# Kernel tuning notes

Hardware: AMD Instinct MI355X
Metric: run time of the kernel (lower is better)

The kernel has to match this reference:

```python
import jax, jax.numpy as jnp
import numpy as np

N_NODES = 50000
N_EDGES = 600000
IN_DIM, HID_DIM, OUT_DIM = 128, 256, 40


def setup_inputs() -> dict:
    key = jax.random.key(0)
    ks = jax.random.split(key, 10)
    x = jax.random.normal(ks[0], (N_NODES, IN_DIM), dtype=jnp.float32)
    edge_index = jax.random.randint(ks[1], (2, N_EDGES), 0, N_NODES, dtype=jnp.int64)
    def lin(k, out_d, in_d):
        s = 1.0 / np.sqrt(in_d)
        return jax.random.uniform(k, (out_d, in_d), jnp.float32, -s, s)
    # SAGEConv: lin_l (on aggregated neighbors, with bias) + lin_r (on self, no bias)
    params = {
        "Wl1": lin(ks[2], HID_DIM, IN_DIM), "bl1": jnp.zeros((HID_DIM,), jnp.float32), "Wr1": lin(ks[3], HID_DIM, IN_DIM),
        "Wl2": lin(ks[4], HID_DIM, HID_DIM), "bl2": jnp.zeros((HID_DIM,), jnp.float32), "Wr2": lin(ks[5], HID_DIM, HID_DIM),
        "Wl3": lin(ks[6], OUT_DIM, HID_DIM), "bl3": jnp.zeros((OUT_DIM,), jnp.float32), "Wr3": lin(ks[7], OUT_DIM, HID_DIM),
    }
    return {"x": x, "edge_index": edge_index, **params}


def _sage_conv(x, src, dst, Wl, bl, Wr):
    # mean-aggregate source features into destination nodes
    n = x.shape[0]
    agg = jax.ops.segment_sum(x[src], dst, num_segments=n)          # [N, d_in]
    cnt = jax.ops.segment_sum(jnp.ones_like(dst, dtype=x.dtype), dst, num_segments=n)
    mean = agg / jnp.maximum(cnt, 1.0)[:, None]
    return mean @ Wl.T + bl + x @ Wr.T


def reference(x, edge_index, Wl1, bl1, Wr1, Wl2, bl2, Wr2, Wl3, bl3, Wr3):
    src, dst = edge_index[0], edge_index[1]
    h = _sage_conv(x, src, dst, Wl1, bl1, Wr1)
    h = jax.nn.relu(h)  # dropout is identity in eval mode
    h = _sage_conv(h, src, dst, Wl2, bl2, Wr2)
    h = jax.nn.relu(h)
    h = _sage_conv(h, src, dst, Wl3, bl3, Wr3)
    return jax.nn.log_softmax(h, axis=1)
```

## Files before the change

### kernel.cpp

```cpp
#include <hip/hip_runtime.h>
#include <hip/hip_bf16.h>

#define IN_DIM 128
#define HID_DIM 256
#define OUT_DIM 40
#define SCAN_CHUNK 2048

typedef __attribute__((ext_vector_type(8))) __bf16 bf16x8;
typedef __attribute__((ext_vector_type(4))) float f32x4;

__device__ inline ushort f2bf(float f) {
    uint u = __builtin_bit_cast(uint, f);
    u = (u + 0x7fff + ((u >> 16) & 1)) >> 16;
    return (ushort)u;
}
__device__ inline float bfl(uint u) { return __builtin_bit_cast(float, u << 16); }
__device__ inline float bfh(uint u) { return __builtin_bit_cast(float, u & 0xffff0000u); }

__global__ __launch_bounds__(256) void cvt_x(const float* __restrict__ in,
                                             ushort* __restrict__ out, int n4) {
    int i = blockIdx.x * 256 + threadIdx.x;
    if (i < n4) {
        float4 v = ((const float4*)in)[i];
        uint2 o;
        o.x = (uint)f2bf(v.x) | ((uint)f2bf(v.y) << 16);
        o.y = (uint)f2bf(v.z) | ((uint)f2bf(v.w) << 16);
        ((uint2*)out)[i] = o;
    }
}

__global__ __launch_bounds__(256) void cvt_w2(const float* __restrict__ wl,
                                              const float* __restrict__ wr,
                                              ushort* __restrict__ ol,
                                              ushort* __restrict__ orr,
                                              int O, int OPAD, int K) {
    int idx = blockIdx.x * 256 + threadIdx.x;
    int tot = OPAD * K;
    if (idx >= tot) return;
    int row = idx / K;
    int col = idx - row * K;
    ushort vl = 0, vr = 0;
    if (row < O) {
        vl = f2bf(wl[row * K + col]);
        vr = f2bf(wr[row * K + col]);
    }
    ol[idx] = vl;
    orr[idx] = vr;
}

__global__ __launch_bounds__(256) void hist_kernel(const int* __restrict__ dst,
                                                   int* __restrict__ cnt, int E) {
    int e = blockIdx.x * 256 + threadIdx.x;
    if (e < E) atomicAdd(&cnt[dst[e]], 1);
}

__global__ __launch_bounds__(256) void scan_pass1(const int* __restrict__ cnt,
                                                  int* __restrict__ bsum, int N) {
    __shared__ int red[256];
    const int base = blockIdx.x * SCAN_CHUNK;
    int s = 0;
    for (int i = threadIdx.x; i < SCAN_CHUNK; i += 256) {
        int idx = base + i;
        if (idx < N) s += cnt[idx];
    }
    red[threadIdx.x] = s;
    __syncthreads();
    for (int o = 128; o > 0; o >>= 1) {
        if (threadIdx.x < o) red[threadIdx.x] += red[threadIdx.x + o];
        __syncthreads();
    }
    if (threadIdx.x == 0) bsum[blockIdx.x] = red[0];
}

__global__ __launch_bounds__(256) void scan_pass2(int* __restrict__ bsum, int B) {
    __shared__ int ls[256];
    const int t = threadIdx.x;
    int v = (t < B) ? bsum[t] : 0;
    ls[t] = v;
    __syncthreads();
    for (int o = 1; o < 256; o <<= 1) {
        int u = (t >= o) ? ls[t - o] : 0;
        __syncthreads();
        ls[t] += u;
        __syncthreads();
    }
    if (t < B) bsum[t] = ls[t] - v;
}

__global__ __launch_bounds__(256) void scan_pass3(const int* __restrict__ cnt,
                                                  const int* __restrict__ bsum,
                                                  int* __restrict__ rowptr,
                                                  int* __restrict__ cursor,
                                                  float* __restrict__ inv, int N, int E) {
    __shared__ int ls[256];
    const int tbase = blockIdx.x * SCAN_CHUNK + threadIdx.x * 8;
    int c[8];
    int s = 0;
#pragma unroll
    for (int j = 0; j < 8; ++j) {
        int idx = tbase + j;
        c[j] = (idx < N) ? cnt[idx] : 0;
        s += c[j];
    }
    ls[threadIdx.x] = s;
    __syncthreads();
    for (int o = 1; o < 256; o <<= 1) {
        int u = (threadIdx.x >= o) ? ls[threadIdx.x - o] : 0;
        __syncthreads();
        ls[threadIdx.x] += u;
        __syncthreads();
    }
    int run = bsum[blockIdx.x] + ls[threadIdx.x] - s;
#pragma unroll
    for (int j = 0; j < 8; ++j) {
        int idx = tbase + j;
        if (idx < N) {
            rowptr[idx] = run;
            cursor[idx] = run;
            inv[idx] = 1.0f / fmaxf((float)c[j], 1.0f);
            run += c[j];
        }
    }
    if (blockIdx.x == 0 && threadIdx.x == 0) rowptr[N] = E;
}

__global__ __launch_bounds__(256) void fill_kernel(const int* __restrict__ src,
                                                   const int* __restrict__ dst,
                                                   int* __restrict__ cursor,
                                                   int* __restrict__ srcs, int E) {
    int e = blockIdx.x * 256 + threadIdx.x;
    if (e < E) {
        int pos = atomicAdd(&cursor[dst[e]], 1);
        srcs[pos] = src[e];
    }
}

template <int D>
__global__ __launch_bounds__(256) void gather_mean_bf(const ushort* __restrict__ feat,
                                                      const int* __restrict__ rowptr,
                                                      const int* __restrict__ srcs,
                                                      const float* __restrict__ inv,
                                                      ushort* __restrict__ out, int N) {
    constexpr int V = D / 64;
    const int wave = threadIdx.x >> 6;
    const int lane = threadIdx.x & 63;
    const int n = blockIdx.x * 4 + wave;
    if (n >= N) return;
    const int beg = rowptr[n];
    const int end = rowptr[n + 1];
    const int col = lane * V;
    float a0 = 0.f, a1 = 0.f, a2 = 0.f, a3 = 0.f;
    int e = beg;
    if constexpr (V == 4) {
        for (; e + 3 < end; e += 4) {
            int s0 = srcs[e], s1 = srcs[e + 1], s2 = srcs[e + 2], s3 = srcs[e + 3];
            uint2 q0 = *(const uint2*)&feat[(long long)s0 * D + col];
            uint2 q1 = *(const uint2*)&feat[(long long)s1 * D + col];
            uint2 q2 = *(const uint2*)&feat[(long long)s2 * D + col];
            uint2 q3 = *(const uint2*)&feat[(long long)s3 * D + col];
            a0 += (bfl(q0.x) + bfl(q1.x)) + (bfl(q2.x) + bfl(q3.x));
            a1 += (bfh(q0.x) + bfh(q1.x)) + (bfh(q2.x) + bfh(q3.x));
            a2 += (bfl(q0.y) + bfl(q1.y)) + (bfl(q2.y) + bfl(q3.y));
            a3 += (bfh(q0.y) + bfh(q1.y)) + (bfh(q2.y) + bfh(q3.y));
        }
        for (; e + 1 < end; e += 2) {
            int s0 = srcs[e], s1 = srcs[e + 1];
            uint2 q0 = *(const uint2*)&feat[(long long)s0 * D + col];
            uint2 q1 = *(const uint2*)&feat[(long long)s1 * D + col];
            a0 += bfl(q0.x) + bfl(q1.x);
            a1 += bfh(q0.x) + bfh(q1.x);
            a2 += bfl(q0.y) + bfl(q1.y);
            a3 += bfh(q0.y) + bfh(q1.y);
        }
        if (e < end) {
            uint2 q0 = *(const uint2*)&feat[(long long)srcs[e] * D + col];
            a0 += bfl(q0.x); a1 += bfh(q0.x); a2 += bfl(q0.y); a3 += bfh(q0.y);
        }
        const float sc = inv[n];
        uint2 o;
        o.x = (uint)f2bf(a0 * sc) | ((uint)f2bf(a1 * sc) << 16);
        o.y = (uint)f2bf(a2 * sc) | ((uint)f2bf(a3 * sc) << 16);
        *(uint2*)&out[(long long)n * D + col] = o;
    } else {
        for (; e + 3 < end; e += 4) {
            int s0 = srcs[e], s1 = srcs[e + 1], s2 = srcs[e + 2], s3 = srcs[e + 3];
            uint q0 = *(const uint*)&feat[(long long)s0 * D + col];
            uint q1 = *(const uint*)&feat[(long long)s1 * D + col];
            uint q2 = *(const uint*)&feat[(long long)s2 * D + col];
            uint q3 = *(const uint*)&feat[(long long)s3 * D + col];
            a0 += (bfl(q0) + bfl(q1)) + (bfl(q2) + bfl(q3));
            a1 += (bfh(q0) + bfh(q1)) + (bfh(q2) + bfh(q3));
        }
        for (; e + 1 < end; e += 2) {
            int s0 = srcs[e], s1 = srcs[e + 1];
            uint q0 = *(const uint*)&feat[(long long)s0 * D + col];
            uint q1 = *(const uint*)&feat[(long long)s1 * D + col];
            a0 += bfl(q0) + bfl(q1);
            a1 += bfh(q0) + bfh(q1);
        }
        if (e < end) {
            uint q0 = *(const uint*)&feat[(long long)srcs[e] * D + col];
            a0 += bfl(q0); a1 += bfh(q0);
        }
        const float sc = inv[n];
        uint o = (uint)f2bf(a0 * sc) | ((uint)f2bf(a1 * sc) << 16);
        *(uint*)&out[(long long)n * D + col] = o;
    }
}

template <int K, bool RELU, bool OUTBF>
__global__ __launch_bounds__(256, 3) void sage_gemm_mfma(const ushort* __restrict__ Amean,
                                                         const ushort* __restrict__ Aself,
                                                         const ushort* __restrict__ Wl,
                                                         const float* __restrict__ bias,
                                                         const ushort* __restrict__ Wr,
                                                         void* __restrict__ outv, int N, int O) {
    constexpr int KP = K + 8;
    constexpr int NK = K / 32;
    __shared__ __align__(16) ushort Ws[64 * KP];

    const int tid = threadIdx.x;
    const int wave = tid >> 6;
    const int lane = tid & 63;
    const int ln = lane & 15;
    const int quad = lane >> 4;
    const int bm0 = blockIdx.x * 128;
    const int bn0 = blockIdx.y * 64;

    int arow[2];
#pragma unroll
    for (int rt = 0; rt < 2; ++rt) {
        int r = bm0 + wave * 32 + rt * 16 + ln;
        arow[rt] = min(r, N - 1);
    }

    f32x4 acc[2][4] = {};

    for (int phase = 0; phase < 2; ++phase) {
        const ushort* __restrict__ A = phase ? Aself : Amean;
        const ushort* __restrict__ W = phase ? Wr : Wl;

        __syncthreads();
#pragma unroll
        for (int i = tid; i < 64 * (K / 8); i += 256) {
            int row = i / (K / 8);
            int c8 = (i % (K / 8)) * 8;
            *(ulonglong2*)&Ws[row * KP + c8] =
                *(const ulonglong2*)&W[(long long)(bn0 + row) * K + c8];
        }
        __syncthreads();

        bf16x8 areg[NK][2];
#pragma unroll
        for (int kk = 0; kk < NK; ++kk)
#pragma unroll
            for (int rt = 0; rt < 2; ++rt)
                areg[kk][rt] = *(const bf16x8*)&A[(long long)arow[rt] * K + kk * 32 + quad * 8];

#pragma unroll
        for (int kk = 0; kk < NK; ++kk) {
#pragma unroll
            for (int ct = 0; ct < 4; ++ct) {
                bf16x8 b = *(const bf16x8*)&Ws[(ct * 16 + ln) * KP + kk * 32 + quad * 8];
#pragma unroll
                for (int rt = 0; rt < 2; ++rt)
                    acc[rt][ct] = __builtin_amdgcn_mfma_f32_16x16x32_bf16(areg[kk][rt], b, acc[rt][ct], 0, 0, 0);
            }
        }
    }

#pragma unroll
    for (int rt = 0; rt < 2; ++rt) {
        int rbase = bm0 + wave * 32 + rt * 16 + quad * 4;
#pragma unroll
        for (int ct = 0; ct < 4; ++ct) {
            int col = bn0 + ct * 16 + ln;
            if (col >= O) continue;
            float bv = bias[col];
#pragma unroll
            for (int r = 0; r < 4; ++r) {
                int row = rbase + r;
                if (row >= N) continue;
                float v = acc[rt][ct][r] + bv;
                if (RELU) v = fmaxf(v, 0.f);
                if (OUTBF)
                    ((ushort*)outv)[(long long)row * O + col] = f2bf(v);
                else
                    ((float*)outv)[(long long)row * O + col] = v;
            }
        }
    }
}

template <int K>
__global__ __launch_bounds__(256, 3) void sage_gemm_pre(const ushort* __restrict__ A0,
                                                        const ushort* __restrict__ Wl,
                                                        const ushort* __restrict__ Wr,
                                                        ushort* __restrict__ P,
                                                        float* __restrict__ S, int N, int O) {
    constexpr int KP = 2 * K + 8;
    constexpr int NK = K / 32;
    __shared__ __align__(16) ushort Ws[48 * KP];

    const int tid = threadIdx.x;
    const int wave = tid >> 6;
    const int lane = tid & 63;
    const int ln = lane & 15;
    const int quad = lane >> 4;
    const int bm0 = blockIdx.x * 64;

    const int arow = min(bm0 + wave * 16 + ln, N - 1);

#pragma unroll
    for (int i = tid; i < 48 * (K / 8); i += 256) {
        int row = i / (K / 8);
        int c8 = (i % (K / 8)) * 8;
        *(ulonglong2*)&Ws[row * KP + c8] =
            *(const ulonglong2*)&Wl[(long long)row * K + c8];
        *(ulonglong2*)&Ws[row * KP + K + c8] =
            *(const ulonglong2*)&Wr[(long long)row * K + c8];
    }
    __syncthreads();

    bf16x8 areg[NK];
#pragma unroll
    for (int kk = 0; kk < NK; ++kk)
        areg[kk] = *(const bf16x8*)&A0[(long long)arow * K + kk * 32 + quad * 8];

#pragma unroll
    for (int phase = 0; phase < 2; ++phase) {
        f32x4 acc[3] = {};
#pragma unroll
        for (int kk = 0; kk < NK; ++kk) {
#pragma unroll
            for (int ct = 0; ct < 3; ++ct) {
                bf16x8 b = *(const bf16x8*)&Ws[(ct * 16 + ln) * KP + phase * K + kk * 32 + quad * 8];
                acc[ct] = __builtin_amdgcn_mfma_f32_16x16x32_bf16(areg[kk], b, acc[ct], 0, 0, 0);
            }
        }
        int rbase = bm0 + wave * 16 + quad * 4;
#pragma unroll
        for (int ct = 0; ct < 3; ++ct) {
            int col = ct * 16 + ln;
            if (col >= O) continue;
#pragma unroll
            for (int r = 0; r < 4; ++r) {
                int row = rbase + r;
                if (row >= N) continue;
                if (phase == 0)
                    P[(long long)row * O + col] = f2bf(acc[ct][r]);
                else
                    S[(long long)row * O + col] = acc[ct][r];
            }
        }
    }
}

__global__ __launch_bounds__(256) void agg_bias_lsm(const ushort* __restrict__ P,
                                                    const float* __restrict__ S,
                                                    const float* __restrict__ bias,
                                                    const int* __restrict__ rowptr,
                                                    const int* __restrict__ srcs,
                                                    const float* __restrict__ inv,
                                                    float* __restrict__ out, int N) {
    const int wave = threadIdx.x >> 6;
    const int lane = threadIdx.x & 63;
    const int n = blockIdx.x * 4 + wave;
    if (n >= N) return;
    const int beg = rowptr[n];
    const int end = rowptr[n + 1];
    const bool act = lane < OUT_DIM;
    const int cidx = act ? lane : 0;

    float acc = 0.f;
    int e = beg;
    for (; e + 3 < end; e += 4) {
        int s0 = srcs[e], s1 = srcs[e + 1], s2 = srcs[e + 2], s3 = srcs[e + 3];
        float v0 = __builtin_bit_cast(float, (uint)P[(long long)s0 * OUT_DIM + cidx] << 16);
        float v1 = __builtin_bit_cast(float, (uint)P[(long long)s1 * OUT_DIM + cidx] << 16);
        float v2 = __builtin_bit_cast(float, (uint)P[(long long)s2 * OUT_DIM + cidx] << 16);
        float v3 = __builtin_bit_cast(float, (uint)P[(long long)s3 * OUT_DIM + cidx] << 16);
        acc += (v0 + v1) + (v2 + v3);
    }
    for (; e < end; ++e)
        acc += __builtin_bit_cast(float, (uint)P[(long long)srcs[e] * OUT_DIM + cidx] << 16);

    float v = act ? (acc * inv[n] + S[(long long)n * OUT_DIM + lane] + bias[lane]) : -INFINITY;
    float m = v;
#pragma unroll
    for (int o = 32; o > 0; o >>= 1) m = fmaxf(m, __shfl_xor(m, o, 64));
    float ex = act ? expf(v - m) : 0.f;
    float sm = ex;
#pragma unroll
    for (int o = 32; o > 0; o >>= 1) sm += __shfl_xor(sm, o, 64);
    float ls = logf(sm);
    if (act) out[(long long)n * OUT_DIM + lane] = v - m - ls;
}

extern "C" void kernel_launch(void* const* d_in, const int* in_sizes, int n_in,
                              void* d_out, int out_size, void* d_ws, size_t ws_size,
                              hipStream_t stream) {
    const float* x   = (const float*)d_in[0];
    const int*   ei  = (const int*)d_in[1];
    const float* Wl1 = (const float*)d_in[2];
    const float* bl1 = (const float*)d_in[3];
    const float* Wr1 = (const float*)d_in[4];
    const float* Wl2 = (const float*)d_in[5];
    const float* bl2 = (const float*)d_in[6];
    const float* Wr2 = (const float*)d_in[7];
    const float* Wl3 = (const float*)d_in[8];
    const float* bl3 = (const float*)d_in[9];
    const float* Wr3 = (const float*)d_in[10];
    float* out = (float*)d_out;

    const int N = in_sizes[0] / IN_DIM;
    const int E = in_sizes[1] / 2;
    const int* src = ei;
    const int* dst = ei + E;

    char* w = (char*)d_ws;
    size_t off = 0;
    auto alloc = [&](size_t bytes) {
        void* p = w + off;
        off = (off + bytes + 255) & ~(size_t)255;
        return p;
    };
    ushort* xb   = (ushort*)alloc((size_t)N * IN_DIM * 2);
    ushort* M    = (ushort*)alloc((size_t)N * HID_DIM * 2);
    ushort* H1   = (ushort*)alloc((size_t)N * HID_DIM * 2);
    ushort* H2   = (ushort*)alloc((size_t)N * HID_DIM * 2);
    ushort* P3   = (ushort*)alloc((size_t)N * OUT_DIM * 2);
    float*  S3   = (float*)alloc((size_t)N * OUT_DIM * 4);
    float*  inv  = (float*)alloc((size_t)N * 4);
    int*    cnt  = (int*)alloc((size_t)N * 4);
    int*    rowptr = (int*)alloc((size_t)(N + 1) * 4);
    int*    cursor = (int*)alloc((size_t)N * 4);
    int*    srcs = (int*)alloc((size_t)E * 4);
    int*    bsum = (int*)alloc(256 * 4);
    ushort* Wl1b = (ushort*)alloc(256 * 128 * 2);
    ushort* Wr1b = (ushort*)alloc(256 * 128 * 2);
    ushort* Wl2b = (ushort*)alloc(256 * 256 * 2);
    ushort* Wr2b = (ushort*)alloc(256 * 256 * 2);
    ushort* Wl3b = (ushort*)alloc(48 * 256 * 2);
    ushort* Wr3b = (ushort*)alloc(48 * 256 * 2);

    cvt_x<<<(N * IN_DIM / 4 + 255) / 256, 256, 0, stream>>>(x, xb, N * IN_DIM / 4);
    cvt_w2<<<(256 * 128 + 255) / 256, 256, 0, stream>>>(Wl1, Wr1, Wl1b, Wr1b, 256, 256, 128);
    cvt_w2<<<(256 * 256 + 255) / 256, 256, 0, stream>>>(Wl2, Wr2, Wl2b, Wr2b, 256, 256, 256);
    cvt_w2<<<(48 * 256 + 255) / 256, 256, 0, stream>>>(Wl3, Wr3, Wl3b, Wr3b, 40, 48, 256);

    const int SB = (N + SCAN_CHUNK - 1) / SCAN_CHUNK;
    hipMemsetAsync(cnt, 0, (size_t)N * sizeof(int), stream);
    hist_kernel<<<(E + 255) / 256, 256, 0, stream>>>(dst, cnt, E);
    scan_pass1<<<SB, 256, 0, stream>>>(cnt, bsum, N);
    scan_pass2<<<1, 256, 0, stream>>>(bsum, SB);
    scan_pass3<<<SB, 256, 0, stream>>>(cnt, bsum, rowptr, cursor, inv, N, E);
    fill_kernel<<<(E + 255) / 256, 256, 0, stream>>>(src, dst, cursor, srcs, E);

    const int gm = (N + 127) / 128;
    const int gg = (N + 3) / 4;

    gather_mean_bf<IN_DIM><<<gg, 256, 0, stream>>>(xb, rowptr, srcs, inv, M, N);
    sage_gemm_mfma<IN_DIM, true, true><<<dim3(gm, 4), 256, 0, stream>>>(
        M, xb, Wl1b, bl1, Wr1b, H1, N, HID_DIM);

    gather_mean_bf<HID_DIM><<<gg, 256, 0, stream>>>(H1, rowptr, srcs, inv, M, N);
    sage_gemm_mfma<HID_DIM, true, true><<<dim3(gm, 4), 256, 0, stream>>>(
        M, H1, Wl2b, bl2, Wr2b, H2, N, HID_DIM);

    sage_gemm_pre<HID_DIM><<<(N + 63) / 64, 256, 0, stream>>>(
        H2, Wl3b, Wr3b, P3, S3, N, OUT_DIM);
    agg_bias_lsm<<<gg, 256, 0, stream>>>(P3, S3, bl3, rowptr, srcs, inv, out, N);
}
```

Measured before the change: 368.5 us.

## Drop LDS weight staging; load MFMA B operands directly from global memory

Both SAGE GEMM kernels stop copying the weight tile into shared memory with barriers. Each lane now reads its B fragments straight from global memory, relying on L1/L2 caching because the weights are small and shared by all blocks. A fragments are loaded per k-step instead of being preloaded into registers. Launch bounds go from 3 to 4 blocks per CU to raise occupancy, at the risk of more scattered global loads and register pressure.

Result: slower. 444.2 us (+20.6%).

```diff
diff --git a/kernel.cpp b/kernel.cpp
--- a/kernel.cpp
+++ b/kernel.cpp
@@ -209,16 +209,13 @@
 }
 
 template <int K, bool RELU, bool OUTBF>
-__global__ __launch_bounds__(256, 3) void sage_gemm_mfma(const ushort* __restrict__ Amean,
+__global__ __launch_bounds__(256, 4) void sage_gemm_mfma(const ushort* __restrict__ Amean,
                                                          const ushort* __restrict__ Aself,
                                                          const ushort* __restrict__ Wl,
                                                          const float* __restrict__ bias,
                                                          const ushort* __restrict__ Wr,
                                                          void* __restrict__ outv, int N, int O) {
-    constexpr int KP = K + 8;
     constexpr int NK = K / 32;
-    __shared__ __align__(16) ushort Ws[64 * KP];
-
     const int tid = threadIdx.x;
     const int wave = tid >> 6;
     const int lane = tid & 63;
@@ -236,35 +233,26 @@
 
     f32x4 acc[2][4] = {};
 
+#pragma unroll
     for (int phase = 0; phase < 2; ++phase) {
         const ushort* __restrict__ A = phase ? Aself : Amean;
         const ushort* __restrict__ W = phase ? Wr : Wl;
-
-        __syncthreads();
-#pragma unroll
-        for (int i = tid; i < 64 * (K / 8); i += 256) {
-            int row = i / (K / 8);
-            int c8 = (i % (K / 8)) * 8;
-            *(ulonglong2*)&Ws[row * KP + c8] =
-                *(const ulonglong2*)&W[(long long)(bn0 + row) * K + c8];
-        }
-        __syncthreads();
-
-        bf16x8 areg[NK][2];
-#pragma unroll
-        for (int kk = 0; kk < NK; ++kk)
-#pragma unroll
-            for (int rt = 0; rt < 2; ++rt)
-                areg[kk][rt] = *(const bf16x8*)&A[(long long)arow[rt] * K + kk * 32 + quad * 8];
+        const ushort* ap0 = &A[(long long)arow[0] * K + quad * 8];
+        const ushort* ap1 = &A[(long long)arow[1] * K + quad * 8];
+        const ushort* wp[4];
+#pragma unroll
+        for (int ct = 0; ct < 4; ++ct)
+            wp[ct] = &W[(long long)(bn0 + ct * 16 + ln) * K + quad * 8];
 
 #pragma unroll
         for (int kk = 0; kk < NK; ++kk) {
+            bf16x8 a0 = *(const bf16x8*)(ap0 + kk * 32);
+            bf16x8 a1 = *(const bf16x8*)(ap1 + kk * 32);
 #pragma unroll
             for (int ct = 0; ct < 4; ++ct) {
-                bf16x8 b = *(const bf16x8*)&Ws[(ct * 16 + ln) * KP + kk * 32 + quad * 8];
-#pragma unroll
-                for (int rt = 0; rt < 2; ++rt)
-                    acc[rt][ct] = __builtin_amdgcn_mfma_f32_16x16x32_bf16(areg[kk][rt], b, acc[rt][ct], 0, 0, 0);
+                bf16x8 b = *(const bf16x8*)(wp[ct] + kk * 32);
+                acc[0][ct] = __builtin_amdgcn_mfma_f32_16x16x32_bf16(a0, b, acc[0][ct], 0, 0, 0);
+                acc[1][ct] = __builtin_amdgcn_mfma_f32_16x16x32_bf16(a1, b, acc[1][ct], 0, 0, 0);
             }
         }
     }
@@ -293,15 +281,12 @@
 }
 
 template <int K>
-__global__ __launch_bounds__(256, 3) void sage_gemm_pre(const ushort* __restrict__ A0,
+__global__ __launch_bounds__(256, 4) void sage_gemm_pre(const ushort* __restrict__ A0,
                                                         const ushort* __restrict__ Wl,
                                                         const ushort* __restrict__ Wr,
                                                         ushort* __restrict__ P,
                                                         float* __restrict__ S, int N, int O) {
-    constexpr int KP = 2 * K + 8;
     constexpr int NK = K / 32;
-    __shared__ __align__(16) ushort Ws[48 * KP];
-
     const int tid = threadIdx.x;
     const int wave = tid >> 6;
     const int lane = tid & 63;
@@ -310,34 +295,27 @@
     const int bm0 = blockIdx.x * 64;
 
     const int arow = min(bm0 + wave * 16 + ln, N - 1);
-
-#pragma unroll
-    for (int i = tid; i < 48 * (K / 8); i += 256) {
-        int row = i / (K / 8);
-        int c8 = (i % (K / 8)) * 8;
-        *(ulonglong2*)&Ws[row * KP + c8] =
-            *(const ulonglong2*)&Wl[(long long)row * K + c8];
-        *(ulonglong2*)&Ws[row * KP + K + c8] =
-            *(const ulonglong2*)&Wr[(long long)row * K + c8];
-    }
-    __syncthreads();
-
-    bf16x8 areg[NK];
-#pragma unroll
-    for (int kk = 0; kk < NK; ++kk)
-        areg[kk] = *(const bf16x8*)&A0[(long long)arow * K + kk * 32 + quad * 8];
+    const ushort* ap = &A0[(long long)arow * K + quad * 8];
 
 #pragma unroll
     for (int phase = 0; phase < 2; ++phase) {
+        const ushort* __restrict__ W = phase ? Wr : Wl;
+        const ushort* wp[3];
+#pragma unroll
+        for (int ct = 0; ct < 3; ++ct)
+            wp[ct] = &W[(long long)(ct * 16 + ln) * K + quad * 8];
+
         f32x4 acc[3] = {};
 #pragma unroll
         for (int kk = 0; kk < NK; ++kk) {
+            bf16x8 a = *(const bf16x8*)(ap + kk * 32);
 #pragma unroll
             for (int ct = 0; ct < 3; ++ct) {
-                bf16x8 b = *(const bf16x8*)&Ws[(ct * 16 + ln) * KP + phase * K + kk * 32 + quad * 8];
-                acc[ct] = __builtin_amdgcn_mfma_f32_16x16x32_bf16(areg[kk], b, acc[ct], 0, 0, 0);
+                bf16x8 b = *(const bf16x8*)(wp[ct] + kk * 32);
+                acc[ct] = __builtin_amdgcn_mfma_f32_16x16x32_bf16(a, b, acc[ct], 0, 0, 0);
             }
         }
+
         int rbase = bm0 + wave * 16 + quad * 4;
 #pragma unroll
         for (int ct = 0; ct < 3; ++ct) {
```

## Widen GEMM column tile to 128 and stage weights in K-halves

Applied to the files above, without the earlier changes.

The main SAGE GEMM now has each block cover 128 output columns instead of 64, which halves the grid's y-dimension. Each block therefore reads the A rows (mean and self features) from global memory half as often. To keep shared memory bounded, weights are staged in two K-halves with extra barriers, and A fragments are loaded per k-chunk instead of being fully preloaded into registers. The pre-GEMM for layer 3 likewise loads A per k-step to cut register pressure. The trade-offs are more accumulators per thread (64 floats), possible occupancy loss, and extra synchronisation.

After: 385.6 us. 1.05x slower.

```diff
diff --git a/kernel.cpp b/kernel.cpp
--- a/kernel.cpp
+++ b/kernel.cpp
@@ -215,9 +215,10 @@
                                                          const float* __restrict__ bias,
                                                          const ushort* __restrict__ Wr,
                                                          void* __restrict__ outv, int N, int O) {
-    constexpr int KP = K + 8;
-    constexpr int NK = K / 32;
-    __shared__ __align__(16) ushort Ws[64 * KP];
+    constexpr int KH = K / 2;
+    constexpr int KP = KH + 8;
+    constexpr int NC = KH / 32;
+    __shared__ __align__(16) ushort Ws[128 * KP];
 
     const int tid = threadIdx.x;
     const int wave = tid >> 6;
@@ -225,7 +226,7 @@
     const int ln = lane & 15;
     const int quad = lane >> 4;
     const int bm0 = blockIdx.x * 128;
-    const int bn0 = blockIdx.y * 64;
+    const int bn0 = blockIdx.y * 128;
 
     int arow[2];
 #pragma unroll
@@ -234,37 +235,34 @@
         arow[rt] = min(r, N - 1);
     }
 
-    f32x4 acc[2][4] = {};
+    f32x4 acc[2][8] = {};
 
     for (int phase = 0; phase < 2; ++phase) {
         const ushort* __restrict__ A = phase ? Aself : Amean;
         const ushort* __restrict__ W = phase ? Wr : Wl;
-
-        __syncthreads();
-#pragma unroll
-        for (int i = tid; i < 64 * (K / 8); i += 256) {
-            int row = i / (K / 8);
-            int c8 = (i % (K / 8)) * 8;
-            *(ulonglong2*)&Ws[row * KP + c8] =
-                *(const ulonglong2*)&W[(long long)(bn0 + row) * K + c8];
-        }
-        __syncthreads();
-
-        bf16x8 areg[NK][2];
-#pragma unroll
-        for (int kk = 0; kk < NK; ++kk)
-#pragma unroll
-            for (int rt = 0; rt < 2; ++rt)
-                areg[kk][rt] = *(const bf16x8*)&A[(long long)arow[rt] * K + kk * 32 + quad * 8];
-
-#pragma unroll
-        for (int kk = 0; kk < NK; ++kk) {
-#pragma unroll
-            for (int ct = 0; ct < 4; ++ct) {
-                bf16x8 b = *(const bf16x8*)&Ws[(ct * 16 + ln) * KP + kk * 32 + quad * 8];
-#pragma unroll
-                for (int rt = 0; rt < 2; ++rt)
-                    acc[rt][ct] = __builtin_amdgcn_mfma_f32_16x16x32_bf16(areg[kk][rt], b, acc[rt][ct], 0, 0, 0);
+#pragma unroll
+        for (int kh = 0; kh < 2; ++kh) {
+            __syncthreads();
+#pragma unroll
+            for (int i = tid; i < 128 * (KH / 8); i += 256) {
+                int row = i / (KH / 8);
+                int c8 = (i % (KH / 8)) * 8;
+                *(ulonglong2*)&Ws[row * KP + c8] =
+                    *(const ulonglong2*)&W[(long long)(bn0 + row) * K + kh * KH + c8];
+            }
+            __syncthreads();
+
+#pragma unroll
+            for (int c = 0; c < NC; ++c) {
+                const int kk = kh * KH + c * 32;
+                bf16x8 a0 = *(const bf16x8*)&A[(long long)arow[0] * K + kk + quad * 8];
+                bf16x8 a1 = *(const bf16x8*)&A[(long long)arow[1] * K + kk + quad * 8];
+#pragma unroll
+                for (int ct = 0; ct < 8; ++ct) {
+                    bf16x8 b = *(const bf16x8*)&Ws[(ct * 16 + ln) * KP + c * 32 + quad * 8];
+                    acc[0][ct] = __builtin_amdgcn_mfma_f32_16x16x32_bf16(a0, b, acc[0][ct], 0, 0, 0);
+                    acc[1][ct] = __builtin_amdgcn_mfma_f32_16x16x32_bf16(a1, b, acc[1][ct], 0, 0, 0);
+                }
             }
         }
     }
@@ -273,7 +271,7 @@
     for (int rt = 0; rt < 2; ++rt) {
         int rbase = bm0 + wave * 32 + rt * 16 + quad * 4;
 #pragma unroll
-        for (int ct = 0; ct < 4; ++ct) {
+        for (int ct = 0; ct < 8; ++ct) {
             int col = bn0 + ct * 16 + ln;
             if (col >= O) continue;
             float bv = bias[col];
@@ -322,20 +320,16 @@
     }
     __syncthreads();
 
-    bf16x8 areg[NK];
-#pragma unroll
-    for (int kk = 0; kk < NK; ++kk)
-        areg[kk] = *(const bf16x8*)&A0[(long long)arow * K + kk * 32 + quad * 8];
-
 #pragma unroll
     for (int phase = 0; phase < 2; ++phase) {
         f32x4 acc[3] = {};
 #pragma unroll
         for (int kk = 0; kk < NK; ++kk) {
+            bf16x8 a = *(const bf16x8*)&A0[(long long)arow * K + kk * 32 + quad * 8];
 #pragma unroll
             for (int ct = 0; ct < 3; ++ct) {
                 bf16x8 b = *(const bf16x8*)&Ws[(ct * 16 + ln) * KP + phase * K + kk * 32 + quad * 8];
-                acc[ct] = __builtin_amdgcn_mfma_f32_16x16x32_bf16(areg[kk], b, acc[ct], 0, 0, 0);
+                acc[ct] = __builtin_amdgcn_mfma_f32_16x16x32_bf16(a, b, acc[ct], 0, 0, 0);
             }
         }
         int rbase = bm0 + wave * 16 + quad * 4;
@@ -461,11 +455,11 @@
     const int gg = (N + 3) / 4;
 
     gather_mean_bf<IN_DIM><<<gg, 256, 0, stream>>>(xb, rowptr, srcs, inv, M, N);
-    sage_gemm_mfma<IN_DIM, true, true><<<dim3(gm, 4), 256, 0, stream>>>(
+    sage_gemm_mfma<IN_DIM, true, true><<<dim3(gm, 2), 256, 0, stream>>>(
         M, xb, Wl1b, bl1, Wr1b, H1, N, HID_DIM);
 
     gather_mean_bf<HID_DIM><<<gg, 256, 0, stream>>>(H1, rowptr, srcs, inv, M, N);
-    sage_gemm_mfma<HID_DIM, true, true><<<dim3(gm, 4), 256, 0, stream>>>(
+    sage_gemm_mfma<HID_DIM, true, true><<<dim3(gm, 2), 256, 0, stream>>>(
         M, H1, Wl2b, bl2, Wr2b, H2, N, HID_DIM);
 
     sage_gemm_pre<HID_DIM><<<(N + 63) / 64, 256, 0, stream>>>(
```

## Split mean-aggregation gather into column chunks for cache locality

Applied to the files above, without the earlier changes.

The neighbor mean-gather is restructured so each block handles 16 nodes over a 32-column (64-byte) slice of the feature row, with the grid covering all column chunks. Because chunks are processed by separate blocks, the gathered working set per chunk is smaller and more likely to stay in L2, trading wide per-lane loads for narrow 4-byte loads and re-reading the edge lists once per chunk. Separately, the final-layer projection GEMM now loads A fragments inside the k loop rather than preloading all of them into registers, which lowers register pressure.

Measured after the change: 413.1 us. +12.1%, slower.

```diff
diff --git a/kernel.cpp b/kernel.cpp
--- a/kernel.cpp
+++ b/kernel.cpp
@@ -136,76 +136,42 @@
 }
 
 template <int D>
-__global__ __launch_bounds__(256) void gather_mean_bf(const ushort* __restrict__ feat,
-                                                      const int* __restrict__ rowptr,
-                                                      const int* __restrict__ srcs,
-                                                      const float* __restrict__ inv,
-                                                      ushort* __restrict__ out, int N) {
-    constexpr int V = D / 64;
-    const int wave = threadIdx.x >> 6;
-    const int lane = threadIdx.x & 63;
-    const int n = blockIdx.x * 4 + wave;
+__global__ __launch_bounds__(256) void gather_mean_chunk(const ushort* __restrict__ feat,
+                                                         const int* __restrict__ rowptr,
+                                                         const int* __restrict__ srcs,
+                                                         const float* __restrict__ inv,
+                                                         ushort* __restrict__ out,
+                                                         int N, int NB) {
+    const int bx = blockIdx.x;
+    const int chunk = bx / NB;
+    const int nb = bx - chunk * NB;
+    const int g = threadIdx.x >> 4;
+    const int gl = threadIdx.x & 15;
+    const int n = nb * 16 + g;
     if (n >= N) return;
     const int beg = rowptr[n];
     const int end = rowptr[n + 1];
-    const int col = lane * V;
-    float a0 = 0.f, a1 = 0.f, a2 = 0.f, a3 = 0.f;
+    const long long cbase = (long long)chunk * 32 + gl * 2;
+
+    float a0 = 0.f, a1 = 0.f;
     int e = beg;
-    if constexpr (V == 4) {
-        for (; e + 3 < end; e += 4) {
-            int s0 = srcs[e], s1 = srcs[e + 1], s2 = srcs[e + 2], s3 = srcs[e + 3];
-            uint2 q0 = *(const uint2*)&feat[(long long)s0 * D + col];
-            uint2 q1 = *(const uint2*)&feat[(long long)s1 * D + col];
-            uint2 q2 = *(const uint2*)&feat[(long long)s2 * D + col];
-            uint2 q3 = *(const uint2*)&feat[(long long)s3 * D + col];
-            a0 += (bfl(q0.x) + bfl(q1.x)) + (bfl(q2.x) + bfl(q3.x));
-            a1 += (bfh(q0.x) + bfh(q1.x)) + (bfh(q2.x) + bfh(q3.x));
-            a2 += (bfl(q0.y) + bfl(q1.y)) + (bfl(q2.y) + bfl(q3.y));
-            a3 += (bfh(q0.y) + bfh(q1.y)) + (bfh(q2.y) + bfh(q3.y));
-        }
-        for (; e + 1 < end; e += 2) {
-            int s0 = srcs[e], s1 = srcs[e + 1];
-            uint2 q0 = *(const uint2*)&feat[(long long)s0 * D + col];
-            uint2 q1 = *(const uint2*)&feat[(long long)s1 * D + col];
-            a0 += bfl(q0.x) + bfl(q1.x);
-            a1 += bfh(q0.x) + bfh(q1.x);
-            a2 += bfl(q0.y) + bfl(q1.y);
-            a3 += bfh(q0.y) + bfh(q1.y);
-        }
-        if (e < end) {
-            uint2 q0 = *(const uint2*)&feat[(long long)srcs[e] * D + col];
-            a0 += bfl(q0.x); a1 += bfh(q0.x); a2 += bfl(q0.y); a3 += bfh(q0.y);
-        }
-        const float sc = inv[n];
-        uint2 o;
-        o.x = (uint)f2bf(a0 * sc) | ((uint)f2bf(a1 * sc) << 16);
-        o.y = (uint)f2bf(a2 * sc) | ((uint)f2bf(a3 * sc) << 16);
-        *(uint2*)&out[(long long)n * D + col] = o;
-    } else {
-        for (; e + 3 < end; e += 4) {
-            int s0 = srcs[e], s1 = srcs[e + 1], s2 = srcs[e + 2], s3 = srcs[e + 3];
-            uint q0 = *(const uint*)&feat[(long long)s0 * D + col];
-            uint q1 = *(const uint*)&feat[(long long)s1 * D + col];
-            uint q2 = *(const uint*)&feat[(long long)s2 * D + col];
-            uint q3 = *(const uint*)&feat[(long long)s3 * D + col];
-            a0 += (bfl(q0) + bfl(q1)) + (bfl(q2) + bfl(q3));
-            a1 += (bfh(q0) + bfh(q1)) + (bfh(q2) + bfh(q3));
-        }
-        for (; e + 1 < end; e += 2) {
-            int s0 = srcs[e], s1 = srcs[e + 1];
-            uint q0 = *(const uint*)&feat[(long long)s0 * D + col];
-            uint q1 = *(const uint*)&feat[(long long)s1 * D + col];
-            a0 += bfl(q0) + bfl(q1);
-            a1 += bfh(q0) + bfh(q1);
-        }
-        if (e < end) {
-            uint q0 = *(const uint*)&feat[(long long)srcs[e] * D + col];
-            a0 += bfl(q0); a1 += bfh(q0);
-        }
-        const float sc = inv[n];
-        uint o = (uint)f2bf(a0 * sc) | ((uint)f2bf(a1 * sc) << 16);
-        *(uint*)&out[(long long)n * D + col] = o;
-    }
+    for (; e + 3 < end; e += 4) {
+        int s0 = srcs[e], s1 = srcs[e + 1], s2 = srcs[e + 2], s3 = srcs[e + 3];
+        uint q0 = *(const uint*)&feat[(long long)s0 * D + cbase];
+        uint q1 = *(const uint*)&feat[(long long)s1 * D + cbase];
+        uint q2 = *(const uint*)&feat[(long long)s2 * D + cbase];
+        uint q3 = *(const uint*)&feat[(long long)s3 * D + cbase];
+        a0 += (bfl(q0) + bfl(q1)) + (bfl(q2) + bfl(q3));
+        a1 += (bfh(q0) + bfh(q1)) + (bfh(q2) + bfh(q3));
+    }
+    for (; e < end; ++e) {
+        uint q = *(const uint*)&feat[(long long)srcs[e] * D + cbase];
+        a0 += bfl(q);
+        a1 += bfh(q);
+    }
+    const float sc = inv[n];
+    uint o = (uint)f2bf(a0 * sc) | ((uint)f2bf(a1 * sc) << 16);
+    *(uint*)&out[(long long)n * D + cbase] = o;
 }
 
 template <int K, bool RELU, bool OUTBF>
@@ -322,20 +288,16 @@
     }
     __syncthreads();
 
-    bf16x8 areg[NK];
-#pragma unroll
-    for (int kk = 0; kk < NK; ++kk)
-        areg[kk] = *(const bf16x8*)&A0[(long long)arow * K + kk * 32 + quad * 8];
-
 #pragma unroll
     for (int phase = 0; phase < 2; ++phase) {
         f32x4 acc[3] = {};
 #pragma unroll
         for (int kk = 0; kk < NK; ++kk) {
+            bf16x8 a = *(const bf16x8*)&A0[(long long)arow * K + kk * 32 + quad * 8];
 #pragma unroll
             for (int ct = 0; ct < 3; ++ct) {
                 bf16x8 b = *(const bf16x8*)&Ws[(ct * 16 + ln) * KP + phase * K + kk * 32 + quad * 8];
-                acc[ct] = __builtin_amdgcn_mfma_f32_16x16x32_bf16(areg[kk], b, acc[ct], 0, 0, 0);
+                acc[ct] = __builtin_amdgcn_mfma_f32_16x16x32_bf16(a, b, acc[ct], 0, 0, 0);
             }
         }
         int rbase = bm0 + wave * 16 + quad * 4;
@@ -459,12 +421,15 @@
 
     const int gm = (N + 127) / 128;
     const int gg = (N + 3) / 4;
-
-    gather_mean_bf<IN_DIM><<<gg, 256, 0, stream>>>(xb, rowptr, srcs, inv, M, N);
+    const int NB = (N + 15) / 16;
+
+    gather_mean_chunk<IN_DIM><<<NB * (IN_DIM / 32), 256, 0, stream>>>(
+        xb, rowptr, srcs, inv, M, N, NB);
     sage_gemm_mfma<IN_DIM, true, true><<<dim3(gm, 4), 256, 0, stream>>>(
         M, xb, Wl1b, bl1, Wr1b, H1, N, HID_DIM);
 
-    gather_mean_bf<HID_DIM><<<gg, 256, 0, stream>>>(H1, rowptr, srcs, inv, M, N);
+    gather_mean_chunk<HID_DIM><<<NB * (HID_DIM / 32), 256, 0, stream>>>(
+        H1, rowptr, srcs, inv, M, N, NB);
     sage_gemm_mfma<HID_DIM, true, true><<<dim3(gm, 4), 256, 0, stream>>>(
         M, H1, Wl2b, bl2, Wr2b, H2, N, HID_DIM);
 
```
